# Optimization experiments

Measured on AMD Instinct MI355X. Metric: run time of the kernel, lower is better.

The kernel has to match this reference:

```python
import jax, jax.numpy as jnp
import numpy as np

B, H, W, C = 32, 56, 56, 192
HEADS = 6
WS = 7            # window size
SS = 3            # shift size
N = WS * WS       # tokens per window (49)
HID = 4 * C
EPS = 1e-5


def _rel_index():
    coords = np.stack(np.meshgrid(np.arange(WS), np.arange(WS), indexing='ij')).reshape(2, -1)
    rel = (coords[:, :, None] - coords[:, None, :]).transpose(1, 2, 0)
    rel[:, :, 0] += WS - 1
    rel[:, :, 1] += WS - 1
    rel[:, :, 0] *= 2 * WS - 1
    return rel.sum(-1)  # [N, N] int


def _attn_mask():
    # shift mask, identical to the torch construction; static -> numpy
    m = np.zeros((H, W))
    cnt = 0
    for hs in (slice(0, -WS), slice(-WS, -SS), slice(-SS, None)):
        for ws in (slice(0, -WS), slice(-WS, -SS), slice(-SS, None)):
            m[hs, ws] = cnt
            cnt += 1
    mw = m.reshape(H // WS, WS, W // WS, WS).transpose(0, 2, 1, 3).reshape(-1, N)  # [nW, N]
    diff = mw[:, None, :] - mw[:, :, None]
    return np.where(diff != 0, -100.0, 0.0).astype(np.float32)  # [nW, N, N]

REL_IDX = jnp.asarray(_rel_index())
ATTN_MASK = jnp.asarray(_attn_mask())


def setup_inputs() -> dict:
    key = jax.random.key(0)
    ks = jax.random.split(key, 16)
    s = 0.02
    return {
        'x': jax.random.normal(ks[0], (B, H, W, C), jnp.float32),
        'norm1_g': jnp.ones((C,), jnp.float32),
        'norm1_b': jnp.zeros((C,), jnp.float32),
        'qkv_w': jax.random.normal(ks[1], (C, 3 * C), jnp.float32) * s,
        'qkv_b': jnp.zeros((3 * C,), jnp.float32),
        'proj_w': jax.random.normal(ks[2], (C, C), jnp.float32) * s,
        'proj_b': jnp.zeros((C,), jnp.float32),
        'bias_table': jax.random.normal(ks[3], ((2 * WS - 1) ** 2, HEADS), jnp.float32) * s,
        'norm2_g': jnp.ones((C,), jnp.float32),
        'norm2_b': jnp.zeros((C,), jnp.float32),
        'fc1_w': jax.random.normal(ks[4], (C, HID), jnp.float32) * s,
        'fc1_b': jnp.zeros((HID,), jnp.float32),
        'fc2_w': jax.random.normal(ks[5], (HID, C), jnp.float32) * s,
        'fc2_b': jnp.zeros((C,), jnp.float32),
    }


def _ln(x, g, b):
    mu = jnp.mean(x, -1, keepdims=True)
    var = jnp.var(x, -1, keepdims=True)
    return (x - mu) * jax.lax.rsqrt(var + EPS) * g + b


def _partition(x):
    # [B,H,W,C] -> [B*nW, N, C]
    return x.reshape(B, H // WS, WS, W // WS, WS, C).transpose(0, 1, 3, 2, 4, 5).reshape(-1, N, C)


def _reverse(w):
    # [B*nW, N, C] -> [B,H,W,C]
    return w.reshape(B, H // WS, W // WS, WS, WS, C).transpose(0, 1, 3, 2, 4, 5).reshape(B, H, W, C)


def reference(x, norm1_g, norm1_b, qkv_w, qkv_b, proj_w, proj_b, bias_table,
              norm2_g, norm2_b, fc1_w, fc1_b, fc2_w, fc2_b):
    hd = C // HEADS
    scale = hd ** -0.5
    sc = x
    h = _ln(x, norm1_g, norm1_b)
    h = jnp.roll(h, (-SS, -SS), (1, 2))
    xw = _partition(h)                                  # [B_, N, C]
    B_ = xw.shape[0]
    qkv = (xw @ qkv_w + qkv_b).reshape(B_, N, 3, HEADS, hd).transpose(2, 0, 3, 1, 4)
    q, k, v = qkv[0], qkv[1], qkv[2]                    # [B_, H, N, hd]
    attn = jnp.einsum('bhnd,bhmd->bhnm', q * scale, k)  # [B_, H, N, N]
    bias = bias_table[REL_IDX.reshape(-1)].reshape(N, N, HEADS).transpose(2, 0, 1)
    attn = attn + bias[None]
    nW = (H // WS) * (W // WS)
    attn = attn.reshape(B, nW, HEADS, N, N) + ATTN_MASK[None, :, None]
    attn = jax.nn.softmax(attn.reshape(-1, HEADS, N, N), axis=-1)
    out = jnp.einsum('bhnm,bhmd->bhnd', attn, v).transpose(0, 2, 1, 3).reshape(B_, N, C)
    out = out @ proj_w + proj_b
    h = _reverse(out)
    h = jnp.roll(h, (SS, SS), (1, 2))
    y = sc + h
    m = _ln(y, norm2_g, norm2_b)
    mlp = jax.nn.gelu(m @ fc1_w + fc1_b, approximate=False) @ fc2_w + fc2_b
    return y + mlp
```

## Files before the change

kernel.cpp:

```cpp
#include <hip/hip_runtime.h>
#include <hip/hip_bf16.h>

typedef __hip_bfloat16 bf16;
typedef float f32x4 __attribute__((ext_vector_type(4)));
typedef short bf16x8 __attribute__((ext_vector_type(8)));
typedef short short4v __attribute__((ext_vector_type(4)));
typedef unsigned int u32;

#define NTOK 100352
#define CC 192
#define HIDN 768

__device__ __forceinline__ float b2f(unsigned short u) {
    union { unsigned int u32v; float f; } x; x.u32v = ((unsigned int)u) << 16; return x.f;
}
__device__ __forceinline__ unsigned short f2b(float f) {
    union { float f; unsigned int u; } x; x.f = f;
    unsigned int r = x.u + 0x7FFF + ((x.u >> 16) & 1);
    return (unsigned short)(r >> 16);
}
__device__ __forceinline__ float gelu_f(float x) {
    return x / (1.0f + __expf(-1.702f * x));
}

typedef __attribute__((address_space(1))) const unsigned char gas_u8;
typedef __attribute__((address_space(3))) unsigned char las_u8;
__device__ __forceinline__ void gload_lds16(const void* g, void* l) {
    __builtin_amdgcn_global_load_lds((gas_u8*)g, (las_u8*)l, 16, 0, 0);
}

__global__ void prep_k(const float* __restrict__ qkv_w, const float* __restrict__ proj_w,
                       const float* __restrict__ fc1_w, const float* __restrict__ fc2_w,
                       const float* __restrict__ btab,
                       bf16* __restrict__ qkvT, bf16* __restrict__ projT,
                       bf16* __restrict__ fc1T, bf16* __restrict__ fc2T,
                       float* __restrict__ bm)
{
    int idx = blockIdx.x * 256 + threadIdx.x;
    if (idx < 110592) {
        int c = idx / 192, r = idx % 192;
        qkvT[idx] = __float2bfloat16(qkv_w[(size_t)r * 576 + c]);
    } else if (idx < 147456) {
        int t = idx - 110592, c = t / 192, r = t % 192;
        projT[t] = __float2bfloat16(proj_w[(size_t)r * 192 + c]);
    } else if (idx < 294912) {
        int t = idx - 147456, c = t / 192, r = t % 192;
        fc1T[t] = __float2bfloat16(fc1_w[(size_t)r * 768 + c]);
    } else if (idx < 442368) {
        int t = idx - 294912, c = t / 768, r = t % 768;
        fc2T[t] = __float2bfloat16(fc2_w[(size_t)r * 192 + c]);
    } else if (idx < 540672) {
        int t = idx - 442368;
        int reg = t & 3, lane = (t >> 2) & 63, tile = (t >> 8) & 15;
        int rest = t >> 12, h = rest % 6, cls = rest / 6;
        int mt = tile >> 2, nt = tile & 3;
        int kk = mt * 16 + (lane >> 4) * 4 + reg;
        int q  = nt * 16 + (lane & 15);
        float v;
        if (kk >= 49 || q >= 49) v = -1e9f;
        else {
            int i1 = q / 7, j1 = q % 7, i2 = kk / 7, j2 = kk % 7;
            v = btab[((i1 - i2 + 6) * 13 + (j1 - j2 + 6)) * 6 + h];
            int hb7 = cls >> 1, wb7 = cls & 1;
            int r1 = (hb7 ? (i1 < 4 ? 1 : 2) : 0) * 3 + (wb7 ? (j1 < 4 ? 1 : 2) : 0);
            int r2 = (hb7 ? (i2 < 4 ? 1 : 2) : 0) * 3 + (wb7 ? (j2 < 4 ? 1 : 2) : 0);
            if (r1 != r2) v -= 100.0f;
        }
        bm[t] = v;
    }
}

template<typename ST, bool GATHER>
__global__ __launch_bounds__(256) void ln_k(const ST* __restrict__ src,
                                            const float* __restrict__ gamma,
                                            const float* __restrict__ beta,
                                            bf16* __restrict__ dst) {
    int wave = threadIdx.x >> 6, lane = threadIdx.x & 63;
    int t = blockIdx.x * 4 + wave;
    size_t srow;
    if (GATHER) {
        int w = t / 49, n = t % 49;
        int b = w >> 6, wl = w & 63, hb = wl >> 3, wb = wl & 7;
        int i = n / 7, j = n % 7;
        int sh = hb * 7 + i + 3; if (sh >= 56) sh -= 56;
        int sw = wb * 7 + j + 3; if (sw >= 56) sw -= 56;
        srow = ((size_t)(b * 56 + sh) * 56 + sw) * CC;
    } else {
        srow = (size_t)t * CC;
    }
    float v[4];
    int c = lane * 4;
    float sum = 0.f, sq = 0.f;
    if (lane < 48) {
        if constexpr (sizeof(ST) == 2) {
            short4v d = *(const short4v*)((const bf16*)src + srow + c);
            #pragma unroll
            for (int q = 0; q < 4; ++q) v[q] = b2f((unsigned short)d[q]);
        } else {
            f32x4 d = *(const f32x4*)((const float*)src + srow + c);
            #pragma unroll
            for (int q = 0; q < 4; ++q) v[q] = d[q];
        }
        #pragma unroll
        for (int q = 0; q < 4; ++q) { sum += v[q]; sq += v[q] * v[q]; }
    }
    #pragma unroll
    for (int off = 1; off < 64; off <<= 1) { sum += __shfl_xor(sum, off); sq += __shfl_xor(sq, off); }
    float mu = sum * (1.0f / 192.0f);
    float var = sq * (1.0f / 192.0f) - mu * mu;
    float rstd = rsqrtf(var + 1e-5f);
    if (lane < 48) {
        f32x4 gg = *(const f32x4*)(gamma + c);
        f32x4 bb = *(const f32x4*)(beta + c);
        short4v o;
        #pragma unroll
        for (int q = 0; q < 4; ++q) {
            float val = (v[q] - mu) * rstd * gg[q] + bb[q];
            o[q] = (short)f2b(val);
        }
        *(short4v*)(dst + (size_t)t * CC + c) = o;
    }
}

template<int EPI>
__global__ __launch_bounds__(512) void gemm_t(
    const bf16* __restrict__ X, const bf16* __restrict__ WT,
    const float* __restrict__ bias, int K, int N,
    bf16* __restrict__ outb, float* __restrict__ outf,
    const bf16* __restrict__ yin)
{
    __shared__ bf16 As[2][256 * 64];
    __shared__ bf16 Bs[2][64 * 64];
    const int tid = threadIdx.x;
    const int w = tid >> 6, lane = tid & 63;
    const int w0 = w & 1, w1 = w >> 1;

    const u32 nwg = gridDim.x * gridDim.y;
    u32 bid = blockIdx.y * gridDim.x + blockIdx.x;
    bid = (bid & 7) * (nwg >> 3) + (bid >> 3);
    const int tn0 = (bid % gridDim.x) * 64;
    const int tm0 = (bid / gridDim.x) * 256;

    const int r16 = lane & 15, g8 = (lane >> 4) * 8;

    const bf16* gA[4];
    const bf16* gB;
    #pragma unroll
    for (int j = 0; j < 4; ++j) {
        int c = (w * 4 + j) * 64 + lane;
        int l = c ^ ((c >> 3) & 7);
        gA[j] = X + (size_t)(tm0 + (c >> 3)) * K + (l & 7) * 8;
    }
    {
        int c = w * 64 + lane;
        int l = c ^ ((c >> 3) & 7);
        gB = WT + (size_t)(tn0 + (c >> 3)) * K + (l & 7) * 8;
    }

    auto stage = [&](int buf, int kk) {
        #pragma unroll
        for (int j = 0; j < 4; ++j)
            gload_lds16(gA[j] + kk, (char*)&As[buf][0] + (size_t)(w * 4 + j) * 1024);
        gload_lds16(gB + kk, (char*)&Bs[buf][0] + (size_t)w * 1024);
    };

    f32x4 acc[4][2] = {};
    const int nt = K >> 6;
    stage(0, 0);
    __syncthreads();
    for (int t = 0; t < nt; ++t) {
        int buf = t & 1;
        if (t + 1 < nt) stage(buf ^ 1, (t + 1) << 6);
        const char* ab = (const char*)&As[buf][0];
        const char* bb_ = (const char*)&Bs[buf][0];
        #pragma unroll
        for (int k32 = 0; k32 < 2; ++k32) {
            int kcolb = k32 * 64 + g8 * 2;
            bf16x8 a[4], b[2];
            #pragma unroll
            for (int m = 0; m < 4; ++m) {
                int row = w1 * 64 + m * 16 + r16;
                int byte = row * 128 + kcolb;
                a[m] = *(const bf16x8*)(ab + (byte ^ ((row & 7) << 4)));
            }
            #pragma unroll
            for (int n = 0; n < 2; ++n) {
                int row = w0 * 32 + n * 16 + r16;
                int byte = row * 128 + kcolb;
                b[n] = *(const bf16x8*)(bb_ + (byte ^ ((row & 7) << 4)));
            }
            #pragma unroll
            for (int m = 0; m < 4; ++m)
                #pragma unroll
                for (int n = 0; n < 2; ++n)
                    acc[m][n] = __builtin_amdgcn_mfma_f32_16x16x32_bf16(a[m], b[n], acc[m][n], 0, 0, 0);
        }
        __syncthreads();
    }

    #pragma unroll
    for (int n = 0; n < 2; ++n) {
        int col = tn0 + w0 * 32 + n * 16 + r16;
        float bv = bias[col];
        #pragma unroll
        for (int m = 0; m < 4; ++m) {
            #pragma unroll
            for (int r = 0; r < 4; ++r) {
                int mm = tm0 + w1 * 64 + m * 16 + (lane >> 4) * 4 + r;
                float val = acc[m][n][r] + bv;
                if (EPI == 2) {
                    outb[(size_t)mm * N + col] = __float2bfloat16(gelu_f(val));
                } else if (EPI == 3) {
                    outf[(size_t)mm * N + col] = val + __bfloat162float(yin[(size_t)mm * N + col]);
                } else {
                    outb[((size_t)(col >> 5) * NTOK + mm) * 32 + (col & 31)] = __float2bfloat16(val);
                }
            }
        }
    }
}

__global__ __launch_bounds__(384) void attn_mp(const bf16* __restrict__ qkv,
                                               const float* __restrict__ bm,
                                               const bf16* __restrict__ pwt,
                                               const float* __restrict__ pbias,
                                               const float* __restrict__ x,
                                               bf16* __restrict__ ybf)
{
    __shared__ char Pl[6][8192];
    __shared__ char Vt[6][4096];
    char* At = &Pl[0][0];
    const int w = blockIdx.x;
    const int h = threadIdx.x >> 6, l = threadIdx.x & 63;
    const int w49 = w * 49;
    const int wl = w & 63;
    const int cls = (((wl >> 3) == 7) ? 2 : 0) + (((wl & 7) == 7) ? 1 : 0);
    const int hi8 = (l >> 4) * 8, lo = l & 15;

    {
        const bf16* vbase = qkv + ((size_t)(12 + h) * NTOK + w49) * 32;
        #pragma unroll
        for (int it = 0; it < 4; ++it) {
            int c = it * 64 + l;
            int kk = c >> 2, off = (c & 3) * 8;
            bf16x8 v = {};
            if (c < 196) v = *(const bf16x8*)(vbase + kk * 32 + off);
            #pragma unroll
            for (int j = 0; j < 8; ++j) {
                int d = off + j;
                int byte = (d * 128 + kk * 2) ^ ((d & 7) << 4);
                *(bf16*)(&Vt[h][0] + byte) = ((const bf16*)&v)[j];
            }
        }
    }

    const bf16* qb = qkv + ((size_t)h * NTOK + w49) * 32 + hi8;
    const bf16* kb = qkv + ((size_t)(6 + h) * NTOK + w49) * 32 + hi8;
    bf16x8 af[4], bf_[4];
    #pragma unroll
    for (int mt = 0; mt < 4; ++mt) af[mt] = *(const bf16x8*)(kb + (size_t)(mt * 16 + lo) * 32);
    #pragma unroll
    for (int ntt = 0; ntt < 4; ++ntt) bf_[ntt] = *(const bf16x8*)(qb + (size_t)(ntt * 16 + lo) * 32);
    f32x4 acc[4][4] = {};
    #pragma unroll
    for (int mt = 0; mt < 4; ++mt)
        #pragma unroll
        for (int ntt = 0; ntt < 4; ++ntt)
            acc[mt][ntt] = __builtin_amdgcn_mfma_f32_16x16x32_bf16(af[mt], bf_[ntt], acc[mt][ntt], 0, 0, 0);

    const float scale = 0.17677669529663689f;
    const float* bmb = bm + ((size_t)(cls * 6 + h) << 4) * 256;
    #pragma unroll
    for (int mt = 0; mt < 4; ++mt)
        #pragma unroll
        for (int ntt = 0; ntt < 4; ++ntt) {
            f32x4 bmv = *(const f32x4*)(bmb + (mt * 4 + ntt) * 256 + l * 4);
            #pragma unroll
            for (int r = 0; r < 4; ++r) acc[mt][ntt][r] = acc[mt][ntt][r] * scale + bmv[r];
        }

    float inv[4], mx[4];
    #pragma unroll
    for (int ntt = 0; ntt < 4; ++ntt) {
        float m_ = -1e30f;
        #pragma unroll
        for (int mt = 0; mt < 4; ++mt)
            #pragma unroll
            for (int r = 0; r < 4; ++r) m_ = fmaxf(m_, acc[mt][ntt][r]);
        m_ = fmaxf(m_, __shfl_xor(m_, 16));
        m_ = fmaxf(m_, __shfl_xor(m_, 32));
        mx[ntt] = m_;
    }
    #pragma unroll
    for (int ntt = 0; ntt < 4; ++ntt) {
        float s_ = 0.f;
        #pragma unroll
        for (int mt = 0; mt < 4; ++mt)
            #pragma unroll
            for (int r = 0; r < 4; ++r) {
                float e = __expf(acc[mt][ntt][r] - mx[ntt]);
                acc[mt][ntt][r] = e;
                s_ += e;
            }
        s_ += __shfl_xor(s_, 16);
        s_ += __shfl_xor(s_, 32);
        inv[ntt] = 1.0f / s_;
    }

    #pragma unroll
    for (int mt = 0; mt < 4; ++mt)
        #pragma unroll
        for (int ntt = 0; ntt < 4; ++ntt)
            #pragma unroll
            for (int rp = 0; rp < 4; rp += 2) {
                u32 pk = (u32)f2b(acc[mt][ntt][rp]) | ((u32)f2b(acc[mt][ntt][rp + 1]) << 16);
                int kk = mt * 16 + (l >> 4) * 4 + rp;
                int q  = ntt * 16 + lo;
                int byte = (q * 128 + kk * 2) ^ ((q & 7) << 4);
                *(u32*)(&Pl[h][0] + byte) = pk;
            }

    f32x4 o[4][2] = {};
    #pragma unroll
    for (int ks = 0; ks < 2; ++ks) {
        int kb_ = (ks * 32 + hi8) * 2;
        bf16x8 pa[4], vb[2];
        #pragma unroll
        for (int qt = 0; qt < 4; ++qt) {
            int row = qt * 16 + lo;
            pa[qt] = *(const bf16x8*)(&Pl[h][0] + ((row * 128 + kb_) ^ ((row & 7) << 4)));
        }
        #pragma unroll
        for (int dt = 0; dt < 2; ++dt) {
            int row = dt * 16 + lo;
            vb[dt] = *(const bf16x8*)(&Vt[h][0] + ((row * 128 + kb_) ^ ((row & 7) << 4)));
        }
        #pragma unroll
        for (int qt = 0; qt < 4; ++qt)
            #pragma unroll
            for (int dt = 0; dt < 2; ++dt)
                o[qt][dt] = __builtin_amdgcn_mfma_f32_16x16x32_bf16(pa[qt], vb[dt], o[qt][dt], 0, 0, 0);
    }

    __syncthreads();
    #pragma unroll
    for (int qt = 0; qt < 4; ++qt)
        #pragma unroll
        for (int r = 0; r < 4; ++r) {
            int qrow = (l >> 4) * 4 + r;
            float iv = __shfl(inv[qt], qrow);
            int q = qt * 16 + qrow;
            #pragma unroll
            for (int dt = 0; dt < 2; ++dt) {
                int d = h * 32 + dt * 16 + lo;
                int byte = q * 512 + ((d * 2) ^ ((q & 7) << 4));
                *(bf16*)(At + byte) = __float2bfloat16(o[qt][dt][r] * iv);
            }
        }
    bf16x8 wp[6][2];
    {
        const bf16* wb0 = pwt + (size_t)(h * 32 + lo) * 192 + hi8;
        const bf16* wb1 = wb0 + (size_t)16 * 192;
        #pragma unroll
        for (int t6 = 0; t6 < 6; ++t6) {
            wp[t6][0] = *(const bf16x8*)(wb0 + t6 * 32);
            wp[t6][1] = *(const bf16x8*)(wb1 + t6 * 32);
        }
    }
    float pb0 = pbias[h * 32 + lo], pb1 = pbias[h * 32 + 16 + lo];
    __syncthreads();

    f32x4 acc2[4][2] = {};
    #pragma unroll
    for (int t6 = 0; t6 < 6; ++t6) {
        int k2b = (t6 * 32 + hi8) * 2;
        bf16x8 am[4];
        #pragma unroll
        for (int mt = 0; mt < 4; ++mt) {
            int q = mt * 16 + lo;
            am[mt] = *(const bf16x8*)(At + q * 512 + (k2b ^ ((q & 7) << 4)));
        }
        #pragma unroll
        for (int mt = 0; mt < 4; ++mt)
            #pragma unroll
            for (int nf = 0; nf < 2; ++nf)
                acc2[mt][nf] = __builtin_amdgcn_mfma_f32_16x16x32_bf16(am[mt], wp[t6][nf], acc2[mt][nf], 0, 0, 0);
    }

    const int b_ = w >> 6, hb = wl >> 3, wb2 = wl & 7;
    #pragma unroll
    for (int mt = 0; mt < 4; ++mt) {
        #pragma unroll
        for (int r = 0; r < 4; ++r) {
            int q = mt * 16 + (l >> 4) * 4 + r;
            if (q < 49) {
                int i = q / 7, j = q % 7;
                int oh = hb * 7 + i + 3; if (oh >= 56) oh -= 56;
                int ow = wb2 * 7 + j + 3; if (ow >= 56) ow -= 56;
                size_t dst = ((size_t)(b_ * 56 + oh) * 56 + ow) * CC;
                int n0 = h * 32 + lo;
                ybf[dst + n0]      = __float2bfloat16(x[dst + n0]      + acc2[mt][0][r] + pb0);
                ybf[dst + n0 + 16] = __float2bfloat16(x[dst + n0 + 16] + acc2[mt][1][r] + pb1);
            }
        }
    }
}

extern "C" void kernel_launch(void* const* d_in, const int* in_sizes, int n_in,
                              void* d_out, int out_size, void* d_ws, size_t ws_size,
                              hipStream_t stream) {
    const float* x      = (const float*)d_in[0];
    const float* n1g    = (const float*)d_in[1];
    const float* n1b    = (const float*)d_in[2];
    const float* qkv_w  = (const float*)d_in[3];
    const float* qkv_b  = (const float*)d_in[4];
    const float* proj_w = (const float*)d_in[5];
    const float* proj_b = (const float*)d_in[6];
    const float* btab   = (const float*)d_in[7];
    const float* n2g    = (const float*)d_in[8];
    const float* n2b    = (const float*)d_in[9];
    const float* fc1_w  = (const float*)d_in[10];
    const float* fc1_b  = (const float*)d_in[11];
    const float* fc2_w  = (const float*)d_in[12];
    const float* fc2_b  = (const float*)d_in[13];

    char* ws = (char*)d_ws;
    const size_t XW_OFF  = 0;
    const size_t QKV_OFF = 38535168;
    const size_t YB_OFF  = 192675840;
    const size_t WT_OFF  = 231211008;
    const size_t BM_OFF  = 232095744;
    if (ws_size < 232488960ull) return;

    bf16* xw   = (bf16*)(ws + XW_OFF);
    bf16* mbuf = (bf16*)(ws + XW_OFF);
    bf16* qkvb = (bf16*)(ws + QKV_OFF);
    bf16* hidb = (bf16*)(ws + QKV_OFF);
    bf16* ybf  = (bf16*)(ws + YB_OFF);
    float* yout = (float*)d_out;
    bf16* wt   = (bf16*)(ws + WT_OFF);
    float* bmt = (float*)(ws + BM_OFF);
    bf16* qkv_wT  = wt;
    bf16* proj_wT = wt + 110592;
    bf16* fc1_wT  = wt + 147456;
    bf16* fc2_wT  = wt + 294912;

    prep_k<<<dim3(2112), 256, 0, stream>>>(qkv_w, proj_w, fc1_w, fc2_w, btab,
                                           qkv_wT, proj_wT, fc1_wT, fc2_wT, bmt);

    ln_k<float, true><<<NTOK / 4, 256, 0, stream>>>(x, n1g, n1b, xw);

    gemm_t<4><<<dim3(9, 392), 512, 0, stream>>>(
        xw, qkv_wT, qkv_b, 192, 576, qkvb, nullptr, nullptr);

    attn_mp<<<dim3(2048), 384, 0, stream>>>(qkvb, bmt, proj_wT, proj_b, x, ybf);

    ln_k<bf16, false><<<NTOK / 4, 256, 0, stream>>>(ybf, n2g, n2b, mbuf);

    gemm_t<2><<<dim3(12, 392), 512, 0, stream>>>(
        mbuf, fc1_wT, fc1_b, 192, 768, hidb, nullptr, nullptr);
    gemm_t<3><<<dim3(3, 392), 512, 0, stream>>>(
        hidb, fc2_wT, fc2_b, 768, 192, nullptr, yout, ybf);
}
```

Measured before the change: 343.6 us.

## Write V pre-transposed from QKV GEMM and load it straight into registers

The QKV GEMM epilogue now writes the V columns into a separate d-major buffer, padded to 56 tokens per window. The attention kernel loads its V MFMA operands directly from that buffer into registers, which removes the LDS transpose (byte-wise scattered shared writes) and the Vt shared array. The LDS swizzle for P and the attention output also gains extra XOR bits to cut bank conflicts. In exchange, the GEMM epilogue does strided 2-byte global stores with poor coalescing, and the padded tokens 49-55 of each window are never written, so the kernel relies on zero probabilities hitting finite leftover data.

New measurement: 375.1 us. +9.2%, slower.

```diff
diff --git a/kernel.cpp b/kernel.cpp
--- a/kernel.cpp
+++ b/kernel.cpp
@@ -10,6 +10,7 @@
 #define NTOK 100352
 #define CC 192
 #define HIDN 768
+#define VT_STRIDE 114688
 
 __device__ __forceinline__ float b2f(unsigned short u) {
     union { unsigned int u32v; float f; } x; x.u32v = ((unsigned int)u) << 16; return x.f;
@@ -21,6 +22,9 @@
 }
 __device__ __forceinline__ float gelu_f(float x) {
     return x / (1.0f + __expf(-1.702f * x));
+}
+__device__ __forceinline__ int swz3(int row) {
+    return ((row & 7) << 4) ^ (((row >> 3) & 3) << 5);
 }
 
 typedef __attribute__((address_space(1))) const unsigned char gas_u8;
@@ -127,7 +131,7 @@
     const bf16* __restrict__ X, const bf16* __restrict__ WT,
     const float* __restrict__ bias, int K, int N,
     bf16* __restrict__ outb, float* __restrict__ outf,
-    const bf16* __restrict__ yin)
+    const bf16* __restrict__ yin, bf16* __restrict__ vt)
 {
     __shared__ bf16 As[2][256 * 64];
     __shared__ bf16 Bs[2][64 * 64];
@@ -213,7 +217,12 @@
                 } else if (EPI == 3) {
                     outf[(size_t)mm * N + col] = val + __bfloat162float(yin[(size_t)mm * N + col]);
                 } else {
-                    outb[((size_t)(col >> 5) * NTOK + mm) * 32 + (col & 31)] = __float2bfloat16(val);
+                    if (col < 384) {
+                        outb[((size_t)(col >> 5) * NTOK + mm) * 32 + (col & 31)] = __float2bfloat16(val);
+                    } else {
+                        int d = col - 384;
+                        vt[(size_t)d * VT_STRIDE + (mm / 49) * 56 + (mm % 49)] = __float2bfloat16(val);
+                    }
                 }
             }
         }
@@ -221,6 +230,7 @@
 }
 
 __global__ __launch_bounds__(384) void attn_mp(const bf16* __restrict__ qkv,
+                                               const bf16* __restrict__ vt,
                                                const float* __restrict__ bm,
                                                const bf16* __restrict__ pwt,
                                                const float* __restrict__ pbias,
@@ -228,7 +238,6 @@
                                                bf16* __restrict__ ybf)
 {
     __shared__ char Pl[6][8192];
-    __shared__ char Vt[6][4096];
     char* At = &Pl[0][0];
     const int w = blockIdx.x;
     const int h = threadIdx.x >> 6, l = threadIdx.x & 63;
@@ -237,21 +246,12 @@
     const int cls = (((wl >> 3) == 7) ? 2 : 0) + (((wl & 7) == 7) ? 1 : 0);
     const int hi8 = (l >> 4) * 8, lo = l & 15;
 
-    {
-        const bf16* vbase = qkv + ((size_t)(12 + h) * NTOK + w49) * 32;
-        #pragma unroll
-        for (int it = 0; it < 4; ++it) {
-            int c = it * 64 + l;
-            int kk = c >> 2, off = (c & 3) * 8;
-            bf16x8 v = {};
-            if (c < 196) v = *(const bf16x8*)(vbase + kk * 32 + off);
-            #pragma unroll
-            for (int j = 0; j < 8; ++j) {
-                int d = off + j;
-                int byte = (d * 128 + kk * 2) ^ ((d & 7) << 4);
-                *(bf16*)(&Vt[h][0] + byte) = ((const bf16*)&v)[j];
-            }
-        }
+    bf16x8 vreg[2][2];
+    #pragma unroll
+    for (int dt = 0; dt < 2; ++dt) {
+        const bf16* vr = vt + (size_t)(h * 32 + dt * 16 + lo) * VT_STRIDE + w * 56 + hi8;
+        vreg[0][dt] = *(const bf16x8*)(vr);
+        vreg[1][dt] = *(const bf16x8*)(vr + 32);
     }
 
     const bf16* qb = qkv + ((size_t)h * NTOK + w49) * 32 + hi8;
@@ -316,7 +316,7 @@
                 u32 pk = (u32)f2b(acc[mt][ntt][rp]) | ((u32)f2b(acc[mt][ntt][rp + 1]) << 16);
                 int kk = mt * 16 + (l >> 4) * 4 + rp;
                 int q  = ntt * 16 + lo;
-                int byte = (q * 128 + kk * 2) ^ ((q & 7) << 4);
+                int byte = q * 128 + ((kk * 2) ^ swz3(q));
                 *(u32*)(&Pl[h][0] + byte) = pk;
             }
 
@@ -324,22 +324,17 @@
     #pragma unroll
     for (int ks = 0; ks < 2; ++ks) {
         int kb_ = (ks * 32 + hi8) * 2;
-        bf16x8 pa[4], vb[2];
+        bf16x8 pa[4];
         #pragma unroll
         for (int qt = 0; qt < 4; ++qt) {
             int row = qt * 16 + lo;
-            pa[qt] = *(const bf16x8*)(&Pl[h][0] + ((row * 128 + kb_) ^ ((row & 7) << 4)));
-        }
-        #pragma unroll
-        for (int dt = 0; dt < 2; ++dt) {
-            int row = dt * 16 + lo;
-            vb[dt] = *(const bf16x8*)(&Vt[h][0] + ((row * 128 + kb_) ^ ((row & 7) << 4)));
+            pa[qt] = *(const bf16x8*)(&Pl[h][0] + row * 128 + (kb_ ^ swz3(row)));
         }
         #pragma unroll
         for (int qt = 0; qt < 4; ++qt)
             #pragma unroll
             for (int dt = 0; dt < 2; ++dt)
-                o[qt][dt] = __builtin_amdgcn_mfma_f32_16x16x32_bf16(pa[qt], vb[dt], o[qt][dt], 0, 0, 0);
+                o[qt][dt] = __builtin_amdgcn_mfma_f32_16x16x32_bf16(pa[qt], vreg[ks][dt], o[qt][dt], 0, 0, 0);
     }
 
     __syncthreads();
@@ -353,7 +348,7 @@
             #pragma unroll
             for (int dt = 0; dt < 2; ++dt) {
                 int d = h * 32 + dt * 16 + lo;
-                int byte = q * 512 + ((d * 2) ^ ((q & 7) << 4));
+                int byte = q * 512 + ((d * 2) ^ swz3(q));
                 *(bf16*)(At + byte) = __float2bfloat16(o[qt][dt][r] * iv);
             }
         }
@@ -378,7 +373,7 @@
         #pragma unroll
         for (int mt = 0; mt < 4; ++mt) {
             int q = mt * 16 + lo;
-            am[mt] = *(const bf16x8*)(At + q * 512 + (k2b ^ ((q & 7) << 4)));
+            am[mt] = *(const bf16x8*)(At + q * 512 + (k2b ^ swz3(q)));
         }
         #pragma unroll
         for (int mt = 0; mt < 4; ++mt)
@@ -427,6 +422,7 @@
     char* ws = (char*)d_ws;
     const size_t XW_OFF  = 0;
     const size_t QKV_OFF = 38535168;
+    const size_t VT_OFF  = 115605504;
     const size_t YB_OFF  = 192675840;
     const size_t WT_OFF  = 231211008;
     const size_t BM_OFF  = 232095744;
@@ -435,6 +431,7 @@
     bf16* xw   = (bf16*)(ws + XW_OFF);
     bf16* mbuf = (bf16*)(ws + XW_OFF);
     bf16* qkvb = (bf16*)(ws + QKV_OFF);
+    bf16* vtb  = (bf16*)(ws + VT_OFF);
     bf16* hidb = (bf16*)(ws + QKV_OFF);
     bf16* ybf  = (bf16*)(ws + YB_OFF);
     float* yout = (float*)d_out;
@@ -451,14 +448,14 @@
     ln_k<float, true><<<NTOK / 4, 256, 0, stream>>>(x, n1g, n1b, xw);
 
     gemm_t<4><<<dim3(9, 392), 512, 0, stream>>>(
-        xw, qkv_wT, qkv_b, 192, 576, qkvb, nullptr, nullptr);
-
-    attn_mp<<<dim3(2048), 384, 0, stream>>>(qkvb, bmt, proj_wT, proj_b, x, ybf);
+        xw, qkv_wT, qkv_b, 192, 576, qkvb, nullptr, nullptr, vtb);
+
+    attn_mp<<<dim3(2048), 384, 0, stream>>>(qkvb, vtb, bmt, proj_wT, proj_b, x, ybf);
 
     ln_k<bf16, false><<<NTOK / 4, 256, 0, stream>>>(ybf, n2g, n2b, mbuf);
 
     gemm_t<2><<<dim3(12, 392), 512, 0, stream>>>(
-        mbuf, fc1_wT, fc1_b, 192, 768, hidb, nullptr, nullptr);
+        mbuf, fc1_wT, fc1_b, 192, 768, hidb, nullptr, nullptr, nullptr);
     gemm_t<3><<<dim3(3, 392), 512, 0, stream>>>(
-        hidb, fc2_wT, fc2_b, 768, 192, nullptr, yout, ybf);
-}
+        hidb, fc2_wT, fc2_b, 768, 192, nullptr, yout, ybf, nullptr);
+}
```
